# Kernel tuning notes

Measured on AMD Instinct MI355X. Metric: run time of the kernel, lower is better.

## Reference

```python
import jax, jax.numpy as jnp
import numpy as np

D_MODEL = 512
N_QUBITS = 10
N_LAYERS = 2
N_TOKENS = 16384
DIM = 2 ** N_QUBITS


def _rx(t):
    c = jnp.cos(t / 2) + 0j
    s = -1j * jnp.sin(t / 2)
    return jnp.stack([jnp.stack([c, s]), jnp.stack([s, c])]).astype(jnp.complex64)


def _ry(t):
    c = jnp.cos(t / 2) + 0j
    s = jnp.sin(t / 2) + 0j
    return jnp.stack([jnp.stack([c, -s]), jnp.stack([s, c])]).astype(jnp.complex64)


def _rz(t):
    z = jnp.zeros((), jnp.complex64)
    return jnp.stack([jnp.stack([jnp.exp(-1j * t / 2), z]),
                      jnp.stack([z, jnp.exp(1j * t / 2)])]).astype(jnp.complex64)


def _apply_1q(state, q, U, n):
    # state: [B, 2^n]; qubit 0 is the most significant bit
    B = state.shape[0]
    s = state.reshape(B, 2 ** q, 2, 2 ** (n - q - 1))
    s = jnp.einsum('ij,bajk->baik', U, s)
    return s.reshape(B, 2 ** n)


def _simulate(psi, rot, ent, n):
    # psi: [B, 2^n] complex64. rot: [L, n, 3]. ent: [L, n-1].
    L = rot.shape[0]
    idx = jnp.arange(2 ** n)
    for l in range(L):
        for q in range(n):
            psi = _apply_1q(psi, q, _rx(rot[l, q, 0]), n)
            psi = _apply_1q(psi, q, _ry(rot[l, q, 1]), n)
            psi = _apply_1q(psi, q, _rz(rot[l, q, 2]), n)
        for i in range(n - 1):  # nearest-neighbor parameterized CZ (controlled-phase)
            q1, q2 = i, i + 1
            both = (((idx >> (n - 1 - q1)) & 1) & ((idx >> (n - 1 - q2)) & 1)) == 1
            phase = jnp.where(both, jnp.exp(1j * ent[l, i].astype(jnp.complex64)),
                              jnp.ones((), jnp.complex64))
            psi = psi * phase
    return psi


def setup_inputs() -> dict:
    key = jax.random.key(0)
    ks = jax.random.split(key, 6)
    return {
        'x': jax.random.normal(ks[0], (N_TOKENS, D_MODEL), jnp.float32),
        'W_in': jax.random.normal(ks[1], (DIM, D_MODEL), jnp.float32) / np.sqrt(D_MODEL),
        'b_in': jnp.zeros((DIM,), jnp.float32),
        'W_out': jax.random.normal(ks[2], (D_MODEL, DIM), jnp.float32) / np.sqrt(DIM),
        'b_out': jnp.zeros((D_MODEL,), jnp.float32),
        'rot': jax.random.normal(ks[3], (N_LAYERS, N_QUBITS, 3), jnp.float32),
        'ent': jax.random.normal(ks[4], (N_LAYERS, N_QUBITS - 1), jnp.float32),
        'ln_w': jnp.ones((D_MODEL,), jnp.float32),
        'ln_b': jnp.zeros((D_MODEL,), jnp.float32),
    }


def reference(x, W_in, b_in, W_out, b_out, rot, ent, ln_w, ln_b):
    n = rot.shape[1]
    # input projection to 2^n amplitudes, then L2-normalize (F.normalize, eps=1e-12)
    xq = x @ W_in.T + b_in
    norm = jnp.maximum(jnp.linalg.norm(xq, axis=-1, keepdims=True), 1e-12)
    psi = (xq / norm).astype(jnp.complex64)
    psi = _simulate(psi, rot, ent, n)
    probs = (psi.real ** 2 + psi.imag ** 2).astype(x.dtype)  # |amp|^2
    out = probs @ W_out.T + b_out
    # LayerNorm(d_model), eps=1e-5
    mu = jnp.mean(out, axis=-1, keepdims=True)
    var = jnp.mean((out - mu) ** 2, axis=-1, keepdims=True)
    return (out - mu) / jnp.sqrt(var + 1e-5) * ln_w + ln_b
```

## Files before the change

kernel.cpp:

```cpp
#include <hip/hip_runtime.h>
#include <cstdint>

#define TOKENS 16384
#define DMODEL 512
#define DIM    1024
#define NQ     10
#define NL     2
#define BM     128
#define BN     128
#define BK     32

typedef __bf16 bf16x8 __attribute__((ext_vector_type(8)));
typedef float  f32x4  __attribute__((ext_vector_type(4)));
typedef unsigned short u16x8 __attribute__((ext_vector_type(8)));

__device__ __forceinline__ float b2f(unsigned short h) {
    union { unsigned u; float f; } v; v.u = ((unsigned)h) << 16; return v.f;
}
__device__ __forceinline__ unsigned short f2b(float f) {
    unsigned u = __builtin_bit_cast(unsigned, f);
    return (unsigned short)((u + 0x7FFFu + ((u >> 16) & 1u)) >> 16);
}
__device__ __forceinline__ float2 cmul(float2 a, float2 b) {
    return make_float2(a.x * b.x - a.y * b.y, a.x * b.y + a.y * b.x);
}
__device__ __forceinline__ float2 cadd(float2 a, float2 b) {
    return make_float2(a.x + b.x, a.y + b.y);
}
__device__ __forceinline__ void async_copy16(const void* g, void* l) {
    __builtin_amdgcn_global_load_lds((const __attribute__((address_space(1))) void*)g,
                                     (__attribute__((address_space(3))) void*)l, 16, 0, 0);
}

__global__ __launch_bounds__(256)
void prep_all_kernel(const float* __restrict__ x,  unsigned short* __restrict__ xb,
                     const float* __restrict__ w2, unsigned short* __restrict__ w2b,
                     const float* __restrict__ W_in, unsigned short* __restrict__ wtT,
                     const float* __restrict__ rot, const float* __restrict__ ent,
                     const float* __restrict__ bin,
                     unsigned short* __restrict__ U, float* __restrict__ b2) {
    const int bid = blockIdx.x;
    const int t = threadIdx.x;

    if (bid < 256) {
        __shared__ float2 Gs[NL * NQ * 4];
        const int lane = t & 63;
        const int c = bid * 4 + (t >> 6);

        if (t < NL * NQ) {
            float tx = rot[t * 3 + 0] * 0.5f;
            float ty = rot[t * 3 + 1] * 0.5f;
            float tz = rot[t * 3 + 2] * 0.5f;
            float cx = cosf(tx), sx = sinf(tx);
            float cy = cosf(ty), sy = sinf(ty);
            float cz = cosf(tz), sz = sinf(tz);
            float2 rx00 = make_float2(cx, 0.f),  rx01 = make_float2(0.f, -sx);
            float2 rx10 = make_float2(0.f, -sx), rx11 = make_float2(cx, 0.f);
            float2 ry00 = make_float2(cy, 0.f),  ry01 = make_float2(-sy, 0.f);
            float2 ry10 = make_float2(sy, 0.f),  ry11 = make_float2(cy, 0.f);
            float2 m00 = cadd(cmul(ry00, rx00), cmul(ry01, rx10));
            float2 m01 = cadd(cmul(ry00, rx01), cmul(ry01, rx11));
            float2 m10 = cadd(cmul(ry10, rx00), cmul(ry11, rx10));
            float2 m11 = cadd(cmul(ry10, rx01), cmul(ry11, rx11));
            float2 e0 = make_float2(cz, -sz), e1 = make_float2(cz, sz);
            Gs[t * 4 + 0] = cmul(e0, m00);
            Gs[t * 4 + 1] = cmul(e0, m01);
            Gs[t * 4 + 2] = cmul(e1, m10);
            Gs[t * 4 + 3] = cmul(e1, m11);
        }
        float ef[NL * (NQ - 1)];
        #pragma unroll
        for (int i = 0; i < NL * (NQ - 1); i++) ef[i] = ent[i];
        __syncthreads();

        float2 amp[16];
        #pragma unroll
        for (int r = 0; r < 16; r++)
            amp[r] = make_float2((lane * 16 + r == c) ? 1.f : 0.f, 0.f);

        #pragma unroll 1
        for (int li = 0; li < NL; li++) {
            const int l = NL - 1 - li;
            #pragma unroll
            for (int r = 0; r < 16; r++) {
                int idx = lane * 16 + r;
                float ang = 0.f;
                #pragma unroll
                for (int q = 0; q < NQ - 1; q++) {
                    int both = ((idx >> (9 - q)) & 1) & ((idx >> (8 - q)) & 1);
                    if (both) ang += ef[l * (NQ - 1) + q];
                }
                amp[r] = cmul(amp[r], make_float2(cosf(ang), sinf(ang)));
            }
            const float2* Gl = Gs + l * NQ * 4;
            #pragma unroll
            for (int qq = 0; qq < NQ; qq++) {
                const int q = 9 - qq;
                float2 u00 = Gl[q * 4 + 0], u10 = Gl[q * 4 + 1];
                float2 u01 = Gl[q * 4 + 2], u11 = Gl[q * 4 + 3];
                if (q >= 6) {
                    const int S = 1 << (9 - q);
                    #pragma unroll
                    for (int r = 0; r < 16; r++) {
                        if (r & S) continue;
                        float2 a = amp[r], b = amp[r + S];
                        float2 n0, n1;
                        n0.x = u00.x * a.x - u00.y * a.y + u01.x * b.x - u01.y * b.y;
                        n0.y = u00.x * a.y + u00.y * a.x + u01.x * b.y + u01.y * b.x;
                        n1.x = u10.x * a.x - u10.y * a.y + u11.x * b.x - u11.y * b.y;
                        n1.y = u10.x * a.y + u10.y * a.x + u11.x * b.y + u11.y * b.x;
                        amp[r] = n0; amp[r + S] = n1;
                    }
                } else {
                    const int mask = 32 >> q;
                    int bit = (lane >> (5 - q)) & 1;
                    float2 ua = bit ? u11 : u00;
                    float2 ub = bit ? u10 : u01;
                    #pragma unroll
                    for (int r = 0; r < 16; r++) {
                        float px = __shfl_xor(amp[r].x, mask, 64);
                        float py = __shfl_xor(amp[r].y, mask, 64);
                        float nx = ua.x * amp[r].x - ua.y * amp[r].y + ub.x * px - ub.y * py;
                        float ny = ua.x * amp[r].y + ua.y * amp[r].x + ub.x * py + ub.y * px;
                        amp[r] = make_float2(nx, ny);
                    }
                }
            }
        }

        float accRe = 0.f, accIm = 0.f;
        #pragma unroll
        for (int i = 0; i < 4; i++) {
            float4 bv = *(const float4*)&bin[lane * 16 + i * 4];
            accRe += amp[i * 4 + 0].x * bv.x + amp[i * 4 + 1].x * bv.y
                   + amp[i * 4 + 2].x * bv.z + amp[i * 4 + 3].x * bv.w;
            accIm += amp[i * 4 + 0].y * bv.x + amp[i * 4 + 1].y * bv.y
                   + amp[i * 4 + 2].y * bv.z + amp[i * 4 + 3].y * bv.w;
        }
        #pragma unroll
        for (int m = 1; m < 64; m <<= 1) {
            accRe += __shfl_xor(accRe, m, 64);
            accIm += __shfl_xor(accIm, m, 64);
        }
        if (lane == 0) { b2[2 * c] = accRe; b2[2 * c + 1] = accIm; }

        u16x8 o0, o1, p0, p1;
        #pragma unroll
        for (int r = 0; r < 8; r++) {
            o0[r] = f2b(amp[r].x);     o1[r] = f2b(amp[r + 8].x);
            p0[r] = f2b(amp[r].y);     p1[r] = f2b(amp[r + 8].y);
        }
        unsigned short* rowRe = U + (size_t)(2 * c) * DIM + lane * 16;
        unsigned short* rowIm = U + (size_t)(2 * c + 1) * DIM + lane * 16;
        *(u16x8*)rowRe = o0; *(u16x8*)(rowRe + 8) = o1;
        *(u16x8*)rowIm = p0; *(u16x8*)(rowIm + 8) = p1;
        return;
    }

    if (bid < 768) {
        __shared__ float tile[32][33];
        const int b2i = bid - 256;
        const int tx = t & 31, ty = t >> 5;
        const int d0 = (b2i & 15) * 32, j0 = (b2i >> 4) * 32;
        #pragma unroll
        for (int i = 0; i < 32; i += 8)
            tile[ty + i][tx] = W_in[(size_t)(j0 + ty + i) * DMODEL + d0 + tx];
        __syncthreads();
        #pragma unroll
        for (int i = 0; i < 32; i += 8)
            wtT[(size_t)(d0 + ty + i) * DIM + j0 + tx] = f2b(tile[tx][ty + i]);
        return;
    }

    const int NX4 = TOKENS * DMODEL / 4;
    const int NW4 = DMODEL * DIM / 4;
    const int total = NX4 + NW4;
    const int stride = 2048 * 256;
    for (int i = (bid - 768) * 256 + t; i < total; i += stride) {
        const float* s; unsigned short* d; int j;
        if (i < NX4) { s = x;  d = xb;  j = i; }
        else         { s = w2; d = w2b; j = i - NX4; }
        float4 v = *(const float4*)&s[(size_t)j * 4];
        ushort4 o;
        o.x = f2b(v.x); o.y = f2b(v.y); o.z = f2b(v.z); o.w = f2b(v.w);
        *(ushort4*)&d[(size_t)j * 4] = o;
    }
}

__global__ __launch_bounds__(256)
void fold_kernel(const unsigned short* __restrict__ A, const unsigned short* __restrict__ B,
                 unsigned short* __restrict__ C) {
    __shared__ unsigned short lds_a[BM * BK];
    __shared__ unsigned short lds_b[BN * BK];
    const int t = threadIdx.x;
    const int wave = t >> 6, lane = t & 63;
    const int wm = wave >> 1, wn = wave & 1;
    const int bm0 = blockIdx.y * BM;
    const int bn0 = blockIdx.x * BN;
    const int K = DIM, N = DMODEL;

    f32x4 acc[4][4] = {};
    const int c0 = t, c1 = t + 256;
    const int r0 = c0 >> 2, g0 = (c0 & 3) ^ ((r0 >> 1) & 3);
    const int r1 = c1 >> 2, g1 = (c1 & 3) ^ ((r1 >> 1) & 3);

    for (int k0 = 0; k0 < K; k0 += BK) {
        async_copy16(A + (size_t)(bm0 + r0) * K + k0 + g0 * 8, (char*)lds_a + wave * 1024);
        async_copy16(A + (size_t)(bm0 + r1) * K + k0 + g1 * 8, (char*)lds_a + wave * 1024 + 4096);
        async_copy16(B + (size_t)(bn0 + r0) * K + k0 + g0 * 8, (char*)lds_b + wave * 1024);
        async_copy16(B + (size_t)(bn0 + r1) * K + k0 + g1 * 8, (char*)lds_b + wave * 1024 + 4096);
        __syncthreads();

        bf16x8 af[4], bfr[4];
        #pragma unroll
        for (int i = 0; i < 4; i++) {
            int row = wm * 64 + i * 16 + (lane & 15);
            int slot = (lane >> 4) ^ ((row >> 1) & 3);
            af[i] = *(const bf16x8*)&lds_a[row * BK + slot * 8];
            int nrow = wn * 64 + i * 16 + (lane & 15);
            int nslot = (lane >> 4) ^ ((nrow >> 1) & 3);
            bfr[i] = *(const bf16x8*)&lds_b[nrow * BK + nslot * 8];
        }
        #pragma unroll
        for (int i = 0; i < 4; i++)
            #pragma unroll
            for (int j = 0; j < 4; j++)
                acc[i][j] = __builtin_amdgcn_mfma_f32_16x16x32_bf16(af[i], bfr[j], acc[i][j], 0, 0, 0);
        __syncthreads();
    }

    #pragma unroll
    for (int i = 0; i < 4; i++)
        #pragma unroll
        for (int j = 0; j < 4; j++) {
            int col = bn0 + wn * 64 + j * 16 + (lane & 15);
            #pragma unroll
            for (int r = 0; r < 4; r++) {
                int row = bm0 + wm * 64 + i * 16 + (lane >> 4) * 4 + r;
                C[(size_t)row * N + col] = f2b(acc[i][j][r]);
            }
        }
}

__global__ __launch_bounds__(256)
void gemm1_kernel(const unsigned short* __restrict__ A, const unsigned short* __restrict__ B,
                  const float* __restrict__ bias, unsigned short* __restrict__ P) {
    const int K = DMODEL;
    __shared__ unsigned short lds_a[BM * BK];
    __shared__ unsigned short lds_b[BN * BK];
    const int t = threadIdx.x;
    const int wave = t >> 6, lane = t & 63;
    const int wm = wave >> 1, wn = wave & 1;
    const int bm0 = blockIdx.x * BM;
    const int bn0 = blockIdx.y * BN;

    f32x4 acc[4][4] = {};
    const int c0 = t, c1 = t + 256;
    const int r0 = c0 >> 2, g0 = (c0 & 3) ^ ((r0 >> 1) & 3);
    const int r1 = c1 >> 2, g1 = (c1 & 3) ^ ((r1 >> 1) & 3);

    for (int k0 = 0; k0 < K; k0 += BK) {
        async_copy16(A + (size_t)(bm0 + r0) * K + k0 + g0 * 8, (char*)lds_a + wave * 1024);
        async_copy16(A + (size_t)(bm0 + r1) * K + k0 + g1 * 8, (char*)lds_a + wave * 1024 + 4096);
        async_copy16(B + (size_t)(bn0 + r0) * K + k0 + g0 * 8, (char*)lds_b + wave * 1024);
        async_copy16(B + (size_t)(bn0 + r1) * K + k0 + g1 * 8, (char*)lds_b + wave * 1024 + 4096);
        __syncthreads();

        bf16x8 af[4], bfr[4];
        #pragma unroll
        for (int i = 0; i < 4; i++) {
            int row = wm * 64 + i * 16 + (lane & 15);
            int slot = (lane >> 4) ^ ((row >> 1) & 3);
            af[i] = *(const bf16x8*)&lds_a[row * BK + slot * 8];
            int nrow = wn * 64 + i * 16 + (lane & 15);
            int nslot = (lane >> 4) ^ ((nrow >> 1) & 3);
            bfr[i] = *(const bf16x8*)&lds_b[nrow * BK + nslot * 8];
        }
        #pragma unroll
        for (int i = 0; i < 4; i++)
            #pragma unroll
            for (int j = 0; j < 4; j++)
                acc[i][j] = __builtin_amdgcn_mfma_f32_16x16x32_bf16(af[i], bfr[j], acc[i][j], 0, 0, 0);
        __syncthreads();
    }

    #pragma unroll
    for (int i = 0; i < 4; i++) {
        #pragma unroll
        for (int j = 0; j < 4; j++) {
            int col = bn0 + wn * 64 + j * 16 + (lane & 15);
            float bv = bias[col];
            #pragma unroll
            for (int r = 0; r < 4; r++) {
                int row = bm0 + wm * 64 + i * 16 + (lane >> 4) * 4 + r;
                float val = acc[i][j][r] + bv;
                float v2 = val * val;
                float v2p = v2 + __shfl_xor(v2, 1, 64);
                if (!(lane & 1))
                    P[(size_t)row * DIM + (col >> 1)] = f2b(v2p);
            }
        }
    }
}

__global__ __launch_bounds__(256)
void gemm2_ln_kernel(const unsigned short* __restrict__ A,
                     const unsigned short* __restrict__ B,
                     const float* __restrict__ bias,
                     const float* __restrict__ lw, const float* __restrict__ lb,
                     float* __restrict__ out) {
    __shared__ unsigned short lds_a[32 * BK];
    __shared__ unsigned short lds_b[512 * BK];
    __shared__ float redS[4][32], redQ[4][32];
    __shared__ float muS[32], rsS[32], n2s[32];
    const int t = threadIdx.x, wave = t >> 6, lane = t & 63;
    const int bm0 = blockIdx.x * 32;

    f32x4 acc[2][8] = {};
    f32x4 accN[2] = {};
    bf16x8 ones;
    #pragma unroll
    for (int r = 0; r < 8; r++) ones[r] = (__bf16)1.0f;

    const int ra = t >> 2, ga = (t & 3) ^ ((ra >> 1) & 3);

    for (int k0 = 0; k0 < DIM; k0 += BK) {
        if (wave < 2)
            async_copy16(A + (size_t)(bm0 + ra) * DIM + k0 + ga * 8,
                         (char*)lds_a + wave * 1024);
        #pragma unroll
        for (int s = 0; s < 8; s++) {
            int c = t + s * 256;
            int r = c >> 2, g = (c & 3) ^ ((r >> 1) & 3);
            async_copy16(B + (size_t)r * DIM + k0 + g * 8,
                         (char*)lds_b + s * 4096 + wave * 1024);
        }
        __syncthreads();

        bf16x8 af[2], bfr[8];
        #pragma unroll
        for (int i = 0; i < 2; i++) {
            int row = i * 16 + (lane & 15);
            int slot = (lane >> 4) ^ ((row >> 1) & 3);
            af[i] = *(const bf16x8*)&lds_a[row * BK + slot * 8];
        }
        #pragma unroll
        for (int j = 0; j < 8; j++) {
            int nrow = wave * 128 + j * 16 + (lane & 15);
            int nslot = (lane >> 4) ^ ((nrow >> 1) & 3);
            bfr[j] = *(const bf16x8*)&lds_b[nrow * BK + nslot * 8];
        }
        #pragma unroll
        for (int i = 0; i < 2; i++)
            #pragma unroll
            for (int j = 0; j < 8; j++)
                acc[i][j] = __builtin_amdgcn_mfma_f32_16x16x32_bf16(af[i], bfr[j], acc[i][j], 0, 0, 0);
        if (wave == 0) {
            #pragma unroll
            for (int i = 0; i < 2; i++)
                accN[i] = __builtin_amdgcn_mfma_f32_16x16x32_bf16(af[i], ones, accN[i], 0, 0, 0);
        }
        __syncthreads();
    }

    if (wave == 0 && (lane & 15) == 0) {
        #pragma unroll
        for (int i = 0; i < 2; i++)
            #pragma unroll
            for (int r = 0; r < 4; r++)
                n2s[i * 16 + (lane >> 4) * 4 + r] = accN[i][r];
    }
    __syncthreads();

    const int colb = wave * 128;
    float nn[8];
    #pragma unroll
    for (int i = 0; i < 2; i++)
        #pragma unroll
        for (int r = 0; r < 4; r++) {
            int rl = i * 16 + (lane >> 4) * 4 + r;
            nn[i * 4 + r] = 1.0f / fmaxf(n2s[rl], 1e-24f);
        }
    float pS[8], pQ[8];
    #pragma unroll
    for (int i = 0; i < 2; i++)
        #pragma unroll
        for (int r = 0; r < 4; r++) {
            float s = 0.f, q = 0.f;
            #pragma unroll
            for (int j = 0; j < 8; j++) {
                int col = colb + j * 16 + (lane & 15);
                float val = acc[i][j][r] * nn[i * 4 + r] + bias[col];
                acc[i][j][r] = val;
                s += val; q += val * val;
            }
            s += __shfl_xor(s, 1, 64); q += __shfl_xor(q, 1, 64);
            s += __shfl_xor(s, 2, 64); q += __shfl_xor(q, 2, 64);
            s += __shfl_xor(s, 4, 64); q += __shfl_xor(q, 4, 64);
            s += __shfl_xor(s, 8, 64); q += __shfl_xor(q, 8, 64);
            pS[i * 4 + r] = s; pQ[i * 4 + r] = q;
        }
    if ((lane & 15) == 0) {
        #pragma unroll
        for (int i = 0; i < 2; i++)
            #pragma unroll
            for (int r = 0; r < 4; r++) {
                int rl = i * 16 + (lane >> 4) * 4 + r;
                redS[wave][rl] = pS[i * 4 + r];
                redQ[wave][rl] = pQ[i * 4 + r];
            }
    }
    __syncthreads();
    if (t < 32) {
        float s = redS[0][t] + redS[1][t] + redS[2][t] + redS[3][t];
        float q = redQ[0][t] + redQ[1][t] + redQ[2][t] + redQ[3][t];
        float mu = s * (1.0f / DMODEL);
        float var = q * (1.0f / DMODEL) - mu * mu;
        muS[t] = mu;
        rsS[t] = rsqrtf(var + 1e-5f);
    }
    __syncthreads();
    #pragma unroll
    for (int i = 0; i < 2; i++)
        #pragma unroll
        for (int j = 0; j < 8; j++) {
            int col = colb + j * 16 + (lane & 15);
            float w = lw[col], bb = lb[col];
            #pragma unroll
            for (int r = 0; r < 4; r++) {
                int rl = i * 16 + (lane >> 4) * 4 + r;
                out[(size_t)(bm0 + rl) * DMODEL + col] =
                    (acc[i][j][r] - muS[rl]) * rsS[rl] * w + bb;
            }
        }
}

extern "C" void kernel_launch(void* const* d_in, const int* in_sizes, int n_in,
                              void* d_out, int out_size, void* d_ws, size_t ws_size,
                              hipStream_t stream) {
    (void)in_sizes; (void)n_in; (void)out_size; (void)ws_size;
    const float* x     = (const float*)d_in[0];
    const float* W_in  = (const float*)d_in[1];
    const float* b_in  = (const float*)d_in[2];
    const float* W_out = (const float*)d_in[3];
    const float* b_out = (const float*)d_in[4];
    const float* rot   = (const float*)d_in[5];
    const float* ent   = (const float*)d_in[6];
    const float* ln_w  = (const float*)d_in[7];
    const float* ln_b  = (const float*)d_in[8];
    float* out = (float*)d_out;

    char* ws = (char*)d_ws;
    unsigned short* p    = (unsigned short*)ws;
    unsigned short* x_bf = (unsigned short*)(ws + 33554432ull);
    unsigned short* wtT  = (unsigned short*)(ws + 50331648ull);
    unsigned short* w2b  = (unsigned short*)(ws + 51380224ull);
    unsigned short* Ucat = (unsigned short*)(ws + 52428800ull);
    unsigned short* W1c  = (unsigned short*)(ws + 56623104ull);
    float*          b2   = (float*)(ws + 58720256ull);

    prep_all_kernel<<<2816, 256, 0, stream>>>(x, x_bf, W_out, w2b, W_in, wtT,
                                              rot, ent, b_in, Ucat, b2);
    fold_kernel<<<dim3(DMODEL / BN, 2 * DIM / BM), 256, 0, stream>>>(Ucat, wtT, W1c);
    gemm1_kernel<<<dim3(TOKENS / BM, 2 * DIM / BN), 256, 0, stream>>>(
        x_bf, W1c, b2, p);
    gemm2_ln_kernel<<<TOKENS / 32, 256, 0, stream>>>(
        p, w2b, b_out, ln_w, ln_b, out);
}
```

Measured before the change: 214.0 us.

## Double-buffer gemm1 LDS with BK=64 and swizzle block order for L2 reuse

```diff
diff --git a/kernel.cpp b/kernel.cpp
--- a/kernel.cpp
+++ b/kernel.cpp
@@ -9,6 +9,7 @@
 #define BM     128
 #define BN     128
 #define BK     32
+#define G1BK   64
 
 typedef __bf16 bf16x8 __attribute__((ext_vector_type(8)));
 typedef float  f32x4  __attribute__((ext_vector_type(4)));
@@ -246,43 +247,71 @@
 void gemm1_kernel(const unsigned short* __restrict__ A, const unsigned short* __restrict__ B,
                   const float* __restrict__ bias, unsigned short* __restrict__ P) {
     const int K = DMODEL;
-    __shared__ unsigned short lds_a[BM * BK];
-    __shared__ unsigned short lds_b[BN * BK];
+    __shared__ unsigned short sm[2 * 16384];
     const int t = threadIdx.x;
     const int wave = t >> 6, lane = t & 63;
     const int wm = wave >> 1, wn = wave & 1;
-    const int bm0 = blockIdx.x * BM;
-    const int bn0 = blockIdx.y * BN;
+
+    const int bid = blockIdx.x;
+    const int swz = (bid & 7) * 256 + (bid >> 3);
+    const int bm0 = (swz >> 4) * BM;
+    const int bn0 = (swz & 15) * BN;
 
     f32x4 acc[4][4] = {};
-    const int c0 = t, c1 = t + 256;
-    const int r0 = c0 >> 2, g0 = (c0 & 3) ^ ((r0 >> 1) & 3);
-    const int r1 = c1 >> 2, g1 = (c1 & 3) ^ ((r1 >> 1) & 3);
-
-    for (int k0 = 0; k0 < K; k0 += BK) {
-        async_copy16(A + (size_t)(bm0 + r0) * K + k0 + g0 * 8, (char*)lds_a + wave * 1024);
-        async_copy16(A + (size_t)(bm0 + r1) * K + k0 + g1 * 8, (char*)lds_a + wave * 1024 + 4096);
-        async_copy16(B + (size_t)(bn0 + r0) * K + k0 + g0 * 8, (char*)lds_b + wave * 1024);
-        async_copy16(B + (size_t)(bn0 + r1) * K + k0 + g1 * 8, (char*)lds_b + wave * 1024 + 4096);
-        __syncthreads();
-
-        bf16x8 af[4], bfr[4];
-        #pragma unroll
-        for (int i = 0; i < 4; i++) {
-            int row = wm * 64 + i * 16 + (lane & 15);
-            int slot = (lane >> 4) ^ ((row >> 1) & 3);
-            af[i] = *(const bf16x8*)&lds_a[row * BK + slot * 8];
-            int nrow = wn * 64 + i * 16 + (lane & 15);
-            int nslot = (lane >> 4) ^ ((nrow >> 1) & 3);
-            bfr[i] = *(const bf16x8*)&lds_b[nrow * BK + nslot * 8];
-        }
-        #pragma unroll
-        for (int i = 0; i < 4; i++)
-            #pragma unroll
-            for (int j = 0; j < 4; j++)
-                acc[i][j] = __builtin_amdgcn_mfma_f32_16x16x32_bf16(af[i], bfr[j], acc[i][j], 0, 0, 0);
-        __syncthreads();
-    }
+
+    int rS[4], gS[4];
+    #pragma unroll
+    for (int s = 0; s < 4; s++) {
+        int c = t + s * 256;
+        rS[s] = c >> 3;
+        gS[s] = (c & 7) ^ (rS[s] & 7);
+    }
+
+    #define G1_STAGE(buf, k0)                                                     \
+        {                                                                         \
+            unsigned short* la_ = sm + (buf) * 16384;                             \
+            unsigned short* lb_ = la_ + 8192;                                     \
+            _Pragma("unroll")                                                     \
+            for (int s = 0; s < 4; s++) {                                         \
+                async_copy16(A + (size_t)(bm0 + rS[s]) * K + (k0) + gS[s] * 8,    \
+                             (char*)la_ + (s * 256 + wave * 64) * 16);            \
+                async_copy16(B + (size_t)(bn0 + rS[s]) * K + (k0) + gS[s] * 8,    \
+                             (char*)lb_ + (s * 256 + wave * 64) * 16);            \
+            }                                                                     \
+        }
+
+    G1_STAGE(0, 0);
+    __syncthreads();
+
+    const int NT = K / G1BK;
+    #pragma unroll 2
+    for (int kt = 0; kt < NT; kt++) {
+        const int cur = kt & 1;
+        if (kt + 1 < NT) G1_STAGE(cur ^ 1, (kt + 1) * G1BK);
+
+        const unsigned short* la = sm + cur * 16384;
+        const unsigned short* lb = la + 8192;
+        #pragma unroll
+        for (int kk = 0; kk < 2; kk++) {
+            bf16x8 af[4], bfr[4];
+            #pragma unroll
+            for (int i = 0; i < 4; i++) {
+                int row = wm * 64 + i * 16 + (lane & 15);
+                int slot = ((lane >> 4) + kk * 4) ^ (row & 7);
+                af[i] = *(const bf16x8*)&la[row * 64 + slot * 8];
+                int nrow = wn * 64 + i * 16 + (lane & 15);
+                int nslot = ((lane >> 4) + kk * 4) ^ (nrow & 7);
+                bfr[i] = *(const bf16x8*)&lb[nrow * 64 + nslot * 8];
+            }
+            #pragma unroll
+            for (int i = 0; i < 4; i++)
+                #pragma unroll
+                for (int j = 0; j < 4; j++)
+                    acc[i][j] = __builtin_amdgcn_mfma_f32_16x16x32_bf16(af[i], bfr[j], acc[i][j], 0, 0, 0);
+        }
+        __syncthreads();
+    }
+    #undef G1_STAGE
 
     #pragma unroll
     for (int i = 0; i < 4; i++) {
@@ -462,8 +491,7 @@
     prep_all_kernel<<<2816, 256, 0, stream>>>(x, x_bf, W_out, w2b, W_in, wtT,
                                               rot, ent, b_in, Ucat, b2);
     fold_kernel<<<dim3(DMODEL / BN, 2 * DIM / BM), 256, 0, stream>>>(Ucat, wtT, W1c);
-    gemm1_kernel<<<dim3(TOKENS / BM, 2 * DIM / BN), 256, 0, stream>>>(
-        x_bf, W1c, b2, p);
+    gemm1_kernel<<<2048, 256, 0, stream>>>(x_bf, W1c, b2, p);
     gemm2_ln_kernel<<<TOKENS / 32, 256, 0, stream>>>(
         p, w2b, b_out, ln_w, ln_b, out);
 }
```

After: 214.0 us. Within noise of the previous version (+0.0%).

## Rewrite gemm1 as 256x256 tile with double-buffered async LDS pipeline

Applied to the files above, without the earlier changes.

```diff
diff --git a/kernel.cpp b/kernel.cpp
--- a/kernel.cpp
+++ b/kernel.cpp
@@ -242,57 +242,95 @@
         }
 }
 
-__global__ __launch_bounds__(256)
+__global__ __launch_bounds__(512, 2)
 void gemm1_kernel(const unsigned short* __restrict__ A, const unsigned short* __restrict__ B,
                   const float* __restrict__ bias, unsigned short* __restrict__ P) {
-    const int K = DMODEL;
-    __shared__ unsigned short lds_a[BM * BK];
-    __shared__ unsigned short lds_b[BN * BK];
+    __shared__ unsigned short sm[2 * 32768];
     const int t = threadIdx.x;
     const int wave = t >> 6, lane = t & 63;
-    const int wm = wave >> 1, wn = wave & 1;
-    const int bm0 = blockIdx.x * BM;
-    const int bn0 = blockIdx.y * BN;
-
-    f32x4 acc[4][4] = {};
-    const int c0 = t, c1 = t + 256;
-    const int r0 = c0 >> 2, g0 = (c0 & 3) ^ ((r0 >> 1) & 3);
-    const int r1 = c1 >> 2, g1 = (c1 & 3) ^ ((r1 >> 1) & 3);
-
-    for (int k0 = 0; k0 < K; k0 += BK) {
-        async_copy16(A + (size_t)(bm0 + r0) * K + k0 + g0 * 8, (char*)lds_a + wave * 1024);
-        async_copy16(A + (size_t)(bm0 + r1) * K + k0 + g1 * 8, (char*)lds_a + wave * 1024 + 4096);
-        async_copy16(B + (size_t)(bn0 + r0) * K + k0 + g0 * 8, (char*)lds_b + wave * 1024);
-        async_copy16(B + (size_t)(bn0 + r1) * K + k0 + g1 * 8, (char*)lds_b + wave * 1024 + 4096);
-        __syncthreads();
-
-        bf16x8 af[4], bfr[4];
-        #pragma unroll
-        for (int i = 0; i < 4; i++) {
-            int row = wm * 64 + i * 16 + (lane & 15);
-            int slot = (lane >> 4) ^ ((row >> 1) & 3);
-            af[i] = *(const bf16x8*)&lds_a[row * BK + slot * 8];
-            int nrow = wn * 64 + i * 16 + (lane & 15);
-            int nslot = (lane >> 4) ^ ((nrow >> 1) & 3);
-            bfr[i] = *(const bf16x8*)&lds_b[nrow * BK + nslot * 8];
-        }
-        #pragma unroll
-        for (int i = 0; i < 4; i++)
-            #pragma unroll
-            for (int j = 0; j < 4; j++)
-                acc[i][j] = __builtin_amdgcn_mfma_f32_16x16x32_bf16(af[i], bfr[j], acc[i][j], 0, 0, 0);
-        __syncthreads();
-    }
-
-    #pragma unroll
-    for (int i = 0; i < 4; i++) {
+    const int wm = wave >> 2, wn = wave & 3;
+    const int laneR = lane & 15;
+
+    const int bid = blockIdx.x;
+    const int swz = (bid & 7) * 64 + (bid >> 3);
+    const int bm0 = (swz >> 3) * 256;
+    const int bn0 = (swz & 7) * 256;
+
+    const int csrc  = (t & 3) ^ ((t >> 3) & 3);
+    const int rowg  = t >> 2;
+    const unsigned aOff0 = (unsigned)(bm0 + rowg) * DMODEL + csrc * 8;
+    const unsigned aOff1 = (unsigned)(bm0 + 128 + rowg) * DMODEL + csrc * 8;
+    const unsigned bOff0 = (unsigned)(bn0 + rowg) * DMODEL + csrc * 8;
+    const unsigned bOff1 = (unsigned)(bn0 + 128 + rowg) * DMODEL + csrc * 8;
+
+    const int slotc = (((lane >> 4) ^ ((lane >> 1) & 3)) & 3) * 8;
+
+    f32x4 acc[8][4] = {};
+
+    #define G1_STAGE(nbuf, kk, kb)                                                 \
+    {                                                                              \
+        unsigned short* d0 = sm + (nbuf) * 32768 + (kk) * 8192 + wave * 512;       \
+        async_copy16(A + aOff0 + (kb) + (kk) * 32, d0);                            \
+        async_copy16(A + aOff1 + (kb) + (kk) * 32, d0 + 4096);                     \
+        async_copy16(B + bOff0 + (kb) + (kk) * 32, d0 + 16384);                    \
+        async_copy16(B + bOff1 + (kb) + (kk) * 32, d0 + 20480);                    \
+    }
+
+    #define G1_COMPUTE(cbuf, kk)                                                   \
+    {                                                                              \
+        const unsigned short* la = sm + (cbuf) * 32768 + (kk) * 8192;              \
+        const unsigned short* lb = la + 16384;                                     \
+        bf16x8 af[8], bfr[4];                                                      \
+        _Pragma("unroll")                                                          \
+        for (int i = 0; i < 8; i++)                                                \
+            af[i] = *(const bf16x8*)&la[(wm * 128 + i * 16 + laneR) * 32 + slotc]; \
+        _Pragma("unroll")                                                          \
+        for (int j = 0; j < 4; j++)                                                \
+            bfr[j] = *(const bf16x8*)&lb[(wn * 64 + j * 16 + laneR) * 32 + slotc]; \
+        __builtin_amdgcn_s_setprio(1);                                             \
+        _Pragma("unroll")                                                          \
+        for (int i = 0; i < 8; i++)                                                \
+            _Pragma("unroll")                                                      \
+            for (int j = 0; j < 4; j++)                                            \
+                acc[i][j] = __builtin_amdgcn_mfma_f32_16x16x32_bf16(af[i], bfr[j], acc[i][j], 0, 0, 0); \
+        __builtin_amdgcn_s_setprio(0);                                             \
+    }
+
+    G1_STAGE(0, 0, 0);
+    G1_STAGE(0, 1, 0);
+    asm volatile("s_waitcnt vmcnt(4)" ::: "memory");
+    asm volatile("s_barrier" ::: "memory");
+
+    #pragma unroll
+    for (int kt = 0; kt < 7; kt++) {
+        const int cur = kt & 1, nxt = cur ^ 1;
+        const unsigned kb = (unsigned)(kt + 1) * 64;
+        G1_STAGE(nxt, 0, kb);
+        G1_COMPUTE(cur, 0);
+        asm volatile("s_waitcnt vmcnt(4)" ::: "memory");
+        asm volatile("s_barrier" ::: "memory");
+        G1_STAGE(nxt, 1, kb);
+        G1_COMPUTE(cur, 1);
+        asm volatile("s_waitcnt vmcnt(4)" ::: "memory");
+        asm volatile("s_barrier" ::: "memory");
+    }
+    G1_COMPUTE(1, 0);
+    asm volatile("s_waitcnt vmcnt(0)" ::: "memory");
+    asm volatile("s_barrier" ::: "memory");
+    G1_COMPUTE(1, 1);
+
+    #undef G1_STAGE
+    #undef G1_COMPUTE
+
+    #pragma unroll
+    for (int i = 0; i < 8; i++) {
         #pragma unroll
         for (int j = 0; j < 4; j++) {
-            int col = bn0 + wn * 64 + j * 16 + (lane & 15);
+            int col = bn0 + wn * 64 + j * 16 + laneR;
             float bv = bias[col];
             #pragma unroll
             for (int r = 0; r < 4; r++) {
-                int row = bm0 + wm * 64 + i * 16 + (lane >> 4) * 4 + r;
+                int row = bm0 + wm * 128 + i * 16 + (lane >> 4) * 4 + r;
                 float val = acc[i][j][r] + bv;
                 float v2 = val * val;
                 float v2p = v2 + __shfl_xor(v2, 1, 64);
@@ -462,8 +500,7 @@
     prep_all_kernel<<<2816, 256, 0, stream>>>(x, x_bf, W_out, w2b, W_in, wtT,
                                               rot, ent, b_in, Ucat, b2);
     fold_kernel<<<dim3(DMODEL / BN, 2 * DIM / BM), 256, 0, stream>>>(Ucat, wtT, W1c);
-    gemm1_kernel<<<dim3(TOKENS / BM, 2 * DIM / BN), 256, 0, stream>>>(
-        x_bf, W1c, b2, p);
+    gemm1_kernel<<<512, 512, 0, stream>>>(x_bf, W1c, b2, p);
     gemm2_ln_kernel<<<TOKENS / 32, 256, 0, stream>>>(
         p, w2b, b_out, ln_w, ln_b, out);
 }
```

Result: slower. 224.3 us (+4.8%).
